# Kernel tuning notes

Measured on AMD Instinct MI355X. Metric: run time of the kernel, lower is better.

Reference implementation:

```python
import jax, jax.numpy as jnp
import numpy as np

NUM_HEADS = 20


def _rope(t, pos):
    """Rotary embedding (ESM style, rotate_half on full head_dim).
    t: (T, h, d), pos: (T,) float32 position within each sequence."""
    d = t.shape[-1]
    inv_freq = 1.0 / (10000.0 ** (jnp.arange(0, d, 2, dtype=jnp.float32) / d))  # (d/2,)
    freqs = pos[:, None] * inv_freq[None, :]          # (T, d/2)
    emb = jnp.concatenate([freqs, freqs], axis=-1)    # (T, d)
    cos = jnp.cos(emb)[:, None, :]                    # (T, 1, d)
    sin = jnp.sin(emb)[:, None, :]
    x1, x2 = jnp.split(t, 2, axis=-1)
    rot = jnp.concatenate([-x2, x1], axis=-1)
    return t * cos + rot * sin


def setup_inputs() -> dict:
    key = jax.random.key(0)
    ks = jax.random.split(key, 8)
    E = 1280
    lengths = np.array([512, 768, 1024, 1024, 1024, 1280, 1280, 1280], dtype=np.int64)
    cu_lens = jnp.asarray(np.concatenate([[0], np.cumsum(lengths)]).astype(np.int32))
    T = int(lengths.sum())  # 8192
    s = (2.0 / (E + E)) ** 0.5  # xavier-ish scale
    return {
        "x": jax.random.normal(ks[0], (T, E), jnp.float32),
        "cu_lens": cu_lens,
        "max_len": 1280,
        "Wq": jax.random.normal(ks[1], (E, E), jnp.float32) * s,
        "bq": jnp.zeros((E,), jnp.float32),
        "Wk": jax.random.normal(ks[2], (E, E), jnp.float32) * s,
        "bk": jnp.zeros((E,), jnp.float32),
        "Wv": jax.random.normal(ks[3], (E, E), jnp.float32) * s,
        "bv": jnp.zeros((E,), jnp.float32),
        "Wo": jax.random.normal(ks[4], (E, E), jnp.float32) * (2.0 ** 0.5) * s,
        "bo": jnp.zeros((E,), jnp.float32),
    }


def reference(x, cu_lens, max_len, Wq, bq, Wk, bk, Wv, bv, Wo, bo):
    T, E = x.shape
    h = NUM_HEADS
    d = E // h
    scale = d ** -0.5
    # fused QKV projections (q pre-scaled, softmax_scale=1 as in the original)
    q = ((x @ Wq.T + bq) * scale).reshape(T, h, d)
    k = (x @ Wk.T + bk).reshape(T, h, d)
    v = (x @ Wv.T + bv).reshape(T, h, d)
    # per-token sequence id and within-sequence position from cu_lens
    t_idx = jnp.arange(T)
    seq_id = jnp.searchsorted(cu_lens, t_idx, side='right') - 1  # (T,)
    pos = t_idx - cu_lens[seq_id]                                # (T,) int
    # rotary on q and k with per-sequence positions
    posf = pos.astype(jnp.float32)
    q = _rope(q, posf)
    k = _rope(k, posf)
    # scatter packed tokens into padded (B, max_len, h, d) layout
    B = cu_lens.shape[0] - 1
    qp = jnp.zeros((B, max_len, h, d), q.dtype).at[seq_id, pos].set(q)
    kp = jnp.zeros((B, max_len, h, d), k.dtype).at[seq_id, pos].set(k)
    vp = jnp.zeros((B, max_len, h, d), v.dtype).at[seq_id, pos].set(v)
    valid = jnp.zeros((B, max_len), bool).at[seq_id, pos].set(True)
    # non-causal attention within each sequence (block-diagonal over packed tokens)
    scores = jnp.einsum('blhd,bmhd->bhlm', qp, kp)
    scores = jnp.where(valid[:, None, None, :], scores, -1e9)
    attn = jax.nn.softmax(scores, axis=-1)
    o = jnp.einsum('bhlm,bmhd->blhd', attn, vp)
    # gather back to packed layout and apply output projection
    out_tok = o[seq_id, pos].reshape(T, E)
    return out_tok @ Wo.T + bo
```

## Files before the change

### kernel.cpp

```cpp
#include <hip/hip_runtime.h>
#include <hip/hip_bf16.h>
#include <cstdint>

#define E_DIM   1280
#define NHEADS  20
#define HDIM    64
#define QKV_LD  3840

typedef __attribute__((ext_vector_type(8))) short bf8_t;
typedef __attribute__((ext_vector_type(4))) short bf4_t;
typedef __attribute__((ext_vector_type(4))) float f4_t;

__device__ __forceinline__ short f2bs(float f) {
    union { __hip_bfloat16 h; short s; } u;
    u.h = __float2bfloat16(f);
    return u.s;
}

__device__ __forceinline__ bf4_t pk4(f4_t s) {
    union { bf4_t v; uint32_t u[2]; } r;
    asm("v_cvt_pk_bf16_f32 %0, %1, %2" : "=v"(r.u[0]) : "v"(s[0]), "v"(s[1]));
    asm("v_cvt_pk_bf16_f32 %0, %1, %2" : "=v"(r.u[1]) : "v"(s[2]), "v"(s[3]));
    return r.v;
}

__device__ __forceinline__ f4_t mfma16x32(bf8_t a, bf8_t b, f4_t c) {
    return __builtin_amdgcn_mfma_f32_16x16x32_bf16(a, b, c, 0, 0, 0);
}
__device__ __forceinline__ f4_t mfma16x16(bf4_t a, bf4_t b, f4_t c) {
    return __builtin_amdgcn_mfma_f32_16x16x16bf16_1k(a, b, c, 0, 0, 0);
}

__device__ __forceinline__ void gl_lds16(const void* g, void* l) {
    auto gp = reinterpret_cast<__attribute__((address_space(1))) unsigned int*>(
        reinterpret_cast<uintptr_t>(g));
    auto lp = reinterpret_cast<__attribute__((address_space(3))) unsigned int*>(
        reinterpret_cast<uintptr_t>(l));
    __builtin_amdgcn_global_load_lds(gp, lp, 16, 0, 0);
}

#define QSCALE 0.18033688011112042f

__device__ __forceinline__ void cvt8(__hip_bfloat16* dst, const float* src, float sc) {
    float4 a = *(const float4*)src;
    float4 b = *(const float4*)(src + 4);
    bf8_t v;
    v[0] = f2bs(a.x * sc); v[1] = f2bs(a.y * sc); v[2] = f2bs(a.z * sc); v[3] = f2bs(a.w * sc);
    v[4] = f2bs(b.x * sc); v[5] = f2bs(b.y * sc); v[6] = f2bs(b.z * sc); v[7] = f2bs(b.w * sc);
    *(bf8_t*)dst = v;
}

__global__ __launch_bounds__(256) void prep_kernel(
    const float* __restrict__ x,
    const float* __restrict__ wq, const float* __restrict__ wk,
    const float* __restrict__ wv, const float* __restrict__ wo,
    const float* __restrict__ bq, const float* __restrict__ bk, const float* __restrict__ bv,
    __hip_bfloat16* __restrict__ xbf, __hip_bfloat16* __restrict__ wqkv,
    __hip_bfloat16* __restrict__ wobf, float* __restrict__ bqkv,
    long nx8, long nw8, long nb8)
{
    long u = (long)blockIdx.x * 256 + threadIdx.x;
    if (u < nx8) { cvt8(xbf + u * 8, x + u * 8, 1.0f); return; }
    u -= nx8;
    if (u < 3 * nw8) {
        long e = u * 8;
        long w1 = nw8 * 8;
        const float* src; float sc;
        if (e < w1)            { src = wq + e;           sc = QSCALE; }
        else if (e < 2 * w1)   { src = wk + (e - w1);    sc = 1.0f; }
        else                   { src = wv + (e - 2*w1);  sc = 1.0f; }
        cvt8(wqkv + e, src, sc);
        return;
    }
    u -= 3 * nw8;
    if (u < nw8) { cvt8(wobf + u * 8, wo + u * 8, 1.0f); return; }
    u -= nw8;
    if (u < nb8) {
        long e = u * 8;
        #pragma unroll
        for (int j = 0; j < 8; j++) {
            long i = e + j;
            float v;
            if (i < E_DIM)           v = bq[i] * QSCALE;
            else if (i < 2 * E_DIM)  v = bk[i - E_DIM];
            else                     v = bv[i - 2 * E_DIM];
            bqkv[i] = v;
        }
    }
}

template<bool BF16_OUT>
__global__ __launch_bounds__(256, 3) void gemm_nt(
    const __hip_bfloat16* __restrict__ A, const __hip_bfloat16* __restrict__ Bw,
    const float* __restrict__ bias, void* __restrict__ Cout,
    int M, int N, int K, int ldc)
{
    __shared__ __align__(16) __hip_bfloat16 As[128 * 32];
    __shared__ __align__(16) __hip_bfloat16 Bs[128 * 32];
    const int t = threadIdx.x;
    const int wv = t >> 6;
    const int ln = t & 63;
    const int m16 = ln & 15, q4 = ln >> 4;
    const int row0 = blockIdx.y * 128, col0 = blockIdx.x * 128;
    const int wm = (wv >> 1) * 64, wn = (wv & 1) * 64;

    f4_t acc[4][4] = {};

    for (int k0 = 0; k0 < K; k0 += 32) {
        #pragma unroll
        for (int i = 0; i < 2; i++) {
            int s = i * 256 + t;
            int r = s >> 2, c = s & 3;
            gl_lds16(A + (size_t)(row0 + r) * K + k0 + c * 8,
                     As + (size_t)(i * 256 + wv * 64) * 8);
        }
        #pragma unroll
        for (int i = 0; i < 2; i++) {
            int s = i * 256 + t;
            int r = s >> 2, c = s & 3;
            gl_lds16(Bw + (size_t)(col0 + r) * K + k0 + c * 8,
                     Bs + (size_t)(i * 256 + wv * 64) * 8);
        }
        __syncthreads();
        bf8_t af[4], bfr[4];
        #pragma unroll
        for (int mt = 0; mt < 4; mt++)
            af[mt] = *(const bf8_t*)&As[(wm + mt * 16 + m16) * 32 + q4 * 8];
        #pragma unroll
        for (int nt = 0; nt < 4; nt++)
            bfr[nt] = *(const bf8_t*)&Bs[(wn + nt * 16 + m16) * 32 + q4 * 8];
        #pragma unroll
        for (int mt = 0; mt < 4; mt++)
            #pragma unroll
            for (int nt = 0; nt < 4; nt++)
                acc[mt][nt] = mfma16x32(af[mt], bfr[nt], acc[mt][nt]);
        __syncthreads();
    }

    #pragma unroll
    for (int nt = 0; nt < 4; nt++) {
        int cg = col0 + wn + nt * 16 + m16;
        float bv = bias[cg];
        #pragma unroll
        for (int mt = 0; mt < 4; mt++) {
            #pragma unroll
            for (int r = 0; r < 4; r++) {
                int rg = row0 + wm + mt * 16 + q4 * 4 + r;
                float v = acc[mt][nt][r] + bv;
                if constexpr (BF16_OUT)
                    ((__hip_bfloat16*)Cout)[(long)rg * ldc + cg] = __float2bfloat16(v);
                else
                    ((float*)Cout)[(long)rg * ldc + cg] = v;
            }
        }
    }
}

__global__ __launch_bounds__(512, 2) void gemm256(
    const __hip_bfloat16* __restrict__ A, const __hip_bfloat16* __restrict__ Bw,
    const float* __restrict__ bias, __hip_bfloat16* __restrict__ Cout,
    __hip_bfloat16* __restrict__ vtout, int Tdim,
    int M, int N, int K, int ldc)
{
    __shared__ __align__(16) __hip_bfloat16 As[2][256 * 64];
    __shared__ __align__(16) __hip_bfloat16 Bs[2][256 * 64];

    const int t = threadIdx.x;
    const int wv = t >> 6, ln = t & 63;
    const int m16 = ln & 15, q4 = ln >> 4;
    const int wr = wv >> 2, wc = wv & 3;

    const int gx = N >> 8;
    const int nwg = gridDim.x;
    const int id = blockIdx.x;
    const int swz = ((nwg & 7) == 0) ? (id & 7) * (nwg >> 3) + (id >> 3) : id;
    const int col0 = (swz % gx) << 8;
    const int row0 = (swz / gx) << 8;

    const int NT = K >> 6;

    auto stage = [&](const __hip_bfloat16* src, __hip_bfloat16* dst) {
        #pragma unroll
        for (int i = 0; i < 4; i++) {
            int s = i * 512 + t;
            int r = s >> 3, c = (s & 7) ^ (r & 7);
            gl_lds16(src + (size_t)r * K + c * 8,
                     (char*)dst + (size_t)(i * 512 + wv * 64) * 16);
        }
    };

    stage(A  + (size_t)row0 * K,      &As[0][0]);
    stage(Bw + (size_t)col0 * K,      &Bs[0][0]);
    if (NT > 1) {
        stage(A  + (size_t)row0 * K + 64, &As[1][0]);
        stage(Bw + (size_t)col0 * K + 64, &Bs[1][0]);
        asm volatile("s_waitcnt vmcnt(8)" ::: "memory");
    } else {
        asm volatile("s_waitcnt vmcnt(0)" ::: "memory");
    }
    __builtin_amdgcn_s_barrier();

    f4_t acc[8][4] = {};

    for (int kt = 0; kt < NT; kt++) {
        const __hip_bfloat16* Ab = &As[kt & 1][0];
        const __hip_bfloat16* Bb = &Bs[kt & 1][0];

        auto lda = [&](const __hip_bfloat16* base, int r, int kc) {
            return *(const bf8_t*)&base[r * 64 + ((((kc << 2) | q4) ^ (r & 7)) << 3)];
        };

        bf8_t afr[4][2], bf0[2][2], bf1[2][2];
        #pragma unroll
        for (int mt = 0; mt < 4; mt++)
            #pragma unroll
            for (int kc = 0; kc < 2; kc++)
                afr[mt][kc] = lda(Ab, wr * 128 + mt * 16 + m16, kc);
        #pragma unroll
        for (int nt = 0; nt < 2; nt++)
            #pragma unroll
            for (int kc = 0; kc < 2; kc++)
                bf0[nt][kc] = lda(Bb, wc * 64 + nt * 16 + m16, kc);

        __builtin_amdgcn_s_setprio(1);
        #pragma unroll
        for (int mt = 0; mt < 4; mt++)
            #pragma unroll
            for (int nt = 0; nt < 2; nt++)
                #pragma unroll
                for (int kc = 0; kc < 2; kc++)
                    acc[mt][nt] = mfma16x32(afr[mt][kc], bf0[nt][kc], acc[mt][nt]);
        __builtin_amdgcn_s_setprio(0);

        #pragma unroll
        for (int nt = 0; nt < 2; nt++)
            #pragma unroll
            for (int kc = 0; kc < 2; kc++)
                bf1[nt][kc] = lda(Bb, wc * 64 + (2 + nt) * 16 + m16, kc);

        __builtin_amdgcn_s_setprio(1);
        #pragma unroll
        for (int mt = 0; mt < 4; mt++)
            #pragma unroll
            for (int nt = 0; nt < 2; nt++)
                #pragma unroll
                for (int kc = 0; kc < 2; kc++)
                    acc[mt][2 + nt] = mfma16x32(afr[mt][kc], bf1[nt][kc], acc[mt][2 + nt]);
        __builtin_amdgcn_s_setprio(0);

        #pragma unroll
        for (int mt = 0; mt < 4; mt++)
            #pragma unroll
            for (int kc = 0; kc < 2; kc++)
                afr[mt][kc] = lda(Ab, wr * 128 + (4 + mt) * 16 + m16, kc);

        __builtin_amdgcn_s_setprio(1);
        #pragma unroll
        for (int mt = 0; mt < 4; mt++)
            #pragma unroll
            for (int nt = 0; nt < 2; nt++)
                #pragma unroll
                for (int kc = 0; kc < 2; kc++)
                    acc[4 + mt][2 + nt] = mfma16x32(afr[mt][kc], bf1[nt][kc], acc[4 + mt][2 + nt]);
        __builtin_amdgcn_s_setprio(0);

        __builtin_amdgcn_s_setprio(1);
        #pragma unroll
        for (int mt = 0; mt < 4; mt++)
            #pragma unroll
            for (int nt = 0; nt < 2; nt++)
                #pragma unroll
                for (int kc = 0; kc < 2; kc++)
                    acc[4 + mt][nt] = mfma16x32(afr[mt][kc], bf0[nt][kc], acc[4 + mt][nt]);
        __builtin_amdgcn_s_setprio(0);

        asm volatile("s_waitcnt lgkmcnt(0)" ::: "memory");
        __builtin_amdgcn_s_barrier();

        if (kt + 2 < NT) {
            stage(A  + (size_t)row0 * K + (size_t)(kt + 2) * 64, &As[kt & 1][0]);
            stage(Bw + (size_t)col0 * K + (size_t)(kt + 2) * 64, &Bs[kt & 1][0]);
        }
        if (kt + 1 < NT) {
            if (kt + 2 < NT)
                asm volatile("s_waitcnt vmcnt(8)" ::: "memory");
            else
                asm volatile("s_waitcnt vmcnt(0)" ::: "memory");
            __builtin_amdgcn_s_barrier();
        }
    }

    if (col0 >= 2 * E_DIM) {
        #pragma unroll
        for (int nt = 0; nt < 4; nt++) {
            int cg = col0 + wc * 64 + nt * 16 + m16;
            float bval = bias[cg];
            int vrow = cg - 2 * E_DIM;
            #pragma unroll
            for (int mt = 0; mt < 8; mt++) {
                int rg0 = row0 + wr * 128 + mt * 16 + q4 * 4;
                f4_t vv;
                #pragma unroll
                for (int r = 0; r < 4; r++) vv[r] = acc[mt][nt][r] + bval;
                *(bf4_t*)&vtout[(long)vrow * Tdim + rg0] = pk4(vv);
            }
        }
    } else {
        #pragma unroll
        for (int nt = 0; nt < 4; nt++) {
            int cg = col0 + wc * 64 + nt * 16 + m16;
            float bval = bias[cg];
            #pragma unroll
            for (int mt = 0; mt < 8; mt++) {
                #pragma unroll
                for (int r = 0; r < 4; r++) {
                    int rg = row0 + wr * 128 + mt * 16 + q4 * 4 + r;
                    Cout[(long)rg * ldc + cg] = __float2bfloat16(acc[mt][nt][r] + bval);
                }
            }
        }
    }
}

__global__ __launch_bounds__(256) void rope_kernel(
    __hip_bfloat16* __restrict__ qkv, const int* __restrict__ cu, int B, int T)
{
    long idx = (long)blockIdx.x * 256 + threadIdx.x;
    int i = idx & 31;
    long r = idx >> 5;
    int h = (int)(r % NHEADS);
    int tok = (int)(r / NHEADS);
    if (tok >= T) return;
    int pos = tok;
    for (int b = 1; b <= B; b++) if (tok >= cu[b]) pos = tok - cu[b];
    float rev = (float)pos * exp2f(-(float)i * 0.41524100558003436f
                                   - 2.6514961294723187f);
    rev = rev - floorf(rev);
    float s, c;
    asm("v_sin_f32 %0, %1" : "=v"(s) : "v"(rev));
    asm("v_cos_f32 %0, %1" : "=v"(c) : "v"(rev));
    long base = (long)tok * QKV_LD + h * HDIM + i;
    {
        float q1 = __bfloat162float(qkv[base]);
        float q2 = __bfloat162float(qkv[base + 32]);
        qkv[base]      = __float2bfloat16(q1 * c - q2 * s);
        qkv[base + 32] = __float2bfloat16(q2 * c + q1 * s);
    }
    {
        long kb = base + E_DIM;
        float k1 = __bfloat162float(qkv[kb]);
        float k2 = __bfloat162float(qkv[kb + 32]);
        qkv[kb]      = __float2bfloat16(k1 * c - k2 * s);
        qkv[kb + 32] = __float2bfloat16(k2 * c + k1 * s);
    }
}

__global__ __launch_bounds__(256, 4) void attn_kernel(
    const __hip_bfloat16* __restrict__ qkv, const __hip_bfloat16* __restrict__ vt,
    const int* __restrict__ cu, __hip_bfloat16* __restrict__ obuf, int B, int T)
{
    __shared__ __align__(16) __hip_bfloat16 Ks[2][64 * 64];
    __shared__ __align__(16) __hip_bfloat16 Vs[2][64 * 64];

    int idx = blockIdx.x;
    int h = idx % NHEADS;
    int gt = idx / NHEADS;
    int b = B - 1, l = 0, seq0 = 0;
    for (; b >= 0; --b) {
        seq0 = cu[b];
        l = cu[b + 1] - seq0;
        int ntile = (l + 127) >> 7;
        if (gt < ntile) break;
        gt -= ntile;
    }
    if (b < 0) return;
    int q0 = gt * 128;
    const int NT = (l + 63) >> 6;

    const int t = threadIdx.x;
    const int wv = t >> 6, ln = t & 63;
    const int m16 = ln & 15, q4 = ln >> 4;

    auto stage_full = [&](int kv0n, int bi) {
        #pragma unroll
        for (int i = 0; i < 2; i++) {
            int s2 = i * 256 + t;
            int key = s2 >> 3, cg = (s2 & 7) ^ (key & 7);
            gl_lds16(qkv + (long)(seq0 + kv0n + key) * QKV_LD + E_DIM + h * HDIM + cg * 8,
                     (char*)&Ks[bi][0] + (size_t)(i * 256 + wv * 64) * 16);
        }
        #pragma unroll
        for (int i = 0; i < 2; i++) {
            int s2 = i * 256 + t;
            int d = s2 >> 3, cg = (s2 & 7) ^ (d & 7);
            gl_lds16(vt + (long)(h * HDIM + d) * T + seq0 + kv0n + cg * 8,
                     (char*)&Vs[bi][0] + (size_t)(i * 256 + wv * 64) * 16);
        }
    };
    auto stage_tail = [&](int kv0n, int bi) {
        #pragma unroll
        for (int i = 0; i < 2; i++) {
            int s2 = i * 256 + t;
            int key = s2 >> 3, c = s2 & 7;
            bf8_t v = (bf8_t)0;
            if (kv0n + key < l)
                v = *(const bf8_t*)(qkv + (long)(seq0 + kv0n + key) * QKV_LD + E_DIM + h * HDIM + c * 8);
            *(bf8_t*)&Ks[bi][key * 64 + (c ^ (key & 7)) * 8] = v;
        }
        #pragma unroll
        for (int i = 0; i < 2; i++) {
            int s2 = i * 256 + t;
            int d = s2 >> 3, c = s2 & 7;
            bf8_t v = (bf8_t)0;
            int tb = kv0n + c * 8;
            #pragma unroll
            for (int u = 0; u < 8; u++)
                if (tb + u < l)
                    v[u] = *(const short*)&vt[(long)(h * HDIM + d) * T + seq0 + tb + u];
            *(bf8_t*)&Vs[bi][d * 64 + (c ^ (d & 7)) * 8] = v;
        }
    };

    if (64 <= l) stage_full(0, 0); else stage_tail(0, 0);

    bf8_t bq[2][2];
    #pragma unroll
    for (int nt = 0; nt < 2; nt++) {
        int qrow = q0 + wv * 32 + nt * 16 + m16;
        #pragma unroll
        for (int kc = 0; kc < 2; kc++) {
            bf8_t v = (bf8_t)0;
            if (qrow < l)
                v = *(const bf8_t*)(qkv + (long)(seq0 + qrow) * QKV_LD + h * HDIM + kc * 32 + q4 * 8);
            bq[nt][kc] = v;
        }
    }

    f4_t oacc[2][4] = {};
    float m_s[2] = {-1e30f, -1e30f};
    float l_s[2] = {0.0f, 0.0f};

    const int ksw0 = (q4 ^ (m16 & 7)) * 8;
    const int ksw1 = ((4 + q4) ^ (m16 & 7)) * 8;

    asm volatile("s_waitcnt vmcnt(0) lgkmcnt(0)" ::: "memory");
    __builtin_amdgcn_s_barrier();

    for (int it = 0; it < NT; ++it) {
        const int kv0 = it << 6;
        const bool full = (kv0 + 64 <= l);
        if (it + 1 < NT) {
            int kvn = kv0 + 64;
            if (kvn + 64 <= l) stage_full(kvn, (it + 1) & 1);
            else stage_tail(kvn, (it + 1) & 1);
        }
        const __hip_bfloat16* Kb = Ks[it & 1];
        const __hip_bfloat16* Vb = Vs[it & 1];

        f4_t S[2][4];
        __builtin_amdgcn_s_setprio(1);
        #pragma unroll
        for (int mt = 0; mt < 4; mt++) {
            const __hip_bfloat16* krow = &Kb[(mt * 16 + m16) * 64];
            bf8_t ak0 = *(const bf8_t*)(krow + ksw0);
            bf8_t ak1 = *(const bf8_t*)(krow + ksw1);
            #pragma unroll
            for (int nt = 0; nt < 2; nt++) {
                f4_t a = {};
                a = mfma16x32(ak0, bq[nt][0], a);
                a = mfma16x32(ak1, bq[nt][1], a);
                S[nt][mt] = a;
            }
        }
        __builtin_amdgcn_s_setprio(0);

        if (!full) {
            #pragma unroll
            for (int mt = 0; mt < 4; mt++) {
                #pragma unroll
                for (int r = 0; r < 4; r++) {
                    bool valid = (kv0 + mt * 16 + q4 * 4 + r) < l;
                    #pragma unroll
                    for (int nt = 0; nt < 2; nt++)
                        if (!valid) S[nt][mt][r] = -1e30f;
                }
            }
        }

        #pragma unroll
        for (int nt = 0; nt < 2; nt++) {
            float pm[4];
            #pragma unroll
            for (int mt = 0; mt < 4; mt++)
                pm[mt] = fmaxf(fmaxf(S[nt][mt][0], S[nt][mt][1]),
                               fmaxf(S[nt][mt][2], S[nt][mt][3]));
            float mx = fmaxf(fmaxf(pm[0], pm[1]), fmaxf(pm[2], pm[3]));
            mx = fmaxf(mx, __shfl_xor(mx, 16));
            mx = fmaxf(mx, __shfl_xor(mx, 32));
            if (!__all(mx - m_s[nt] <= 8.0f)) {
                float mn = fmaxf(m_s[nt], mx);
                float al = exp2f(m_s[nt] - mn);
                m_s[nt] = mn;
                l_s[nt] *= al;
                #pragma unroll
                for (int dt = 0; dt < 4; dt++)
                    #pragma unroll
                    for (int r = 0; r < 4; r++)
                        oacc[nt][dt][r] *= al;
            }
            float mcur = m_s[nt];
            float ps[4];
            #pragma unroll
            for (int mt = 0; mt < 4; mt++) {
                f4_t p;
                p[0] = exp2f(S[nt][mt][0] - mcur);
                p[1] = exp2f(S[nt][mt][1] - mcur);
                p[2] = exp2f(S[nt][mt][2] - mcur);
                p[3] = exp2f(S[nt][mt][3] - mcur);
                S[nt][mt] = p;
                ps[mt] = (p[0] + p[1]) + (p[2] + p[3]);
            }
            l_s[nt] += (ps[0] + ps[1]) + (ps[2] + ps[3]);
        }

        __builtin_amdgcn_s_setprio(1);
        #pragma unroll
        for (int mt = 0; mt < 4; mt++) {
            bf4_t bp0 = pk4(S[0][mt]);
            bf4_t bp1 = pk4(S[1][mt]);
            const int vsw = ((mt * 2 + (q4 >> 1)) ^ (m16 & 7)) * 8 + (q4 & 1) * 4;
            #pragma unroll
            for (int dt = 0; dt < 4; dt++) {
                bf4_t av = *(const bf4_t*)&Vb[(dt * 16 + m16) * 64 + vsw];
                oacc[0][dt] = mfma16x16(av, bp0, oacc[0][dt]);
                oacc[1][dt] = mfma16x16(av, bp1, oacc[1][dt]);
            }
        }
        __builtin_amdgcn_s_setprio(0);

        if (it + 1 < NT) {
            asm volatile("s_waitcnt vmcnt(0) lgkmcnt(0)" ::: "memory");
            __builtin_amdgcn_s_barrier();
        }
    }

    #pragma unroll
    for (int nt = 0; nt < 2; nt++) {
        float ls = l_s[nt];
        ls += __shfl_xor(ls, 16);
        ls += __shfl_xor(ls, 32);
        float inv = 1.0f / ls;
        int qrow = q0 + wv * 32 + nt * 16 + m16;
        if (qrow < l) {
            #pragma unroll
            for (int dt = 0; dt < 4; dt++) {
                f4_t o;
                #pragma unroll
                for (int r = 0; r < 4; r++)
                    o[r] = oacc[nt][dt][r] * inv;
                *(bf4_t*)&obuf[(long)(seq0 + qrow) * E_DIM + h * HDIM + dt * 16 + q4 * 4] = pk4(o);
            }
        }
    }
}

extern "C" void kernel_launch(void* const* d_in, const int* in_sizes, int n_in,
                              void* d_out, int out_size, void* d_ws, size_t ws_size,
                              hipStream_t stream) {
    const int E = E_DIM;
    const int T = in_sizes[0] / E;
    const int B = in_sizes[1] - 1;

    const float* x  = (const float*)d_in[0];
    const int*   cu = (const int*)d_in[1];
    const float* Wq = (const float*)d_in[3];
    const float* bq = (const float*)d_in[4];
    const float* Wk = (const float*)d_in[5];
    const float* bk = (const float*)d_in[6];
    const float* Wv = (const float*)d_in[7];
    const float* bv = (const float*)d_in[8];
    const float* Wo = (const float*)d_in[9];
    const float* bo = (const float*)d_in[10];

    char* ws = (char*)d_ws;
    size_t off = 0;
    auto alloc = [&](size_t bytes) -> void* {
        void* p = ws + off;
        off = (off + bytes + 255) & ~(size_t)255;
        return p;
    };
    __hip_bfloat16* xbf   = (__hip_bfloat16*)alloc((size_t)T * E * 2);
    __hip_bfloat16* wqkv  = (__hip_bfloat16*)alloc((size_t)3 * E * E * 2);
    __hip_bfloat16* wobf  = (__hip_bfloat16*)alloc((size_t)E * E * 2);
    float*          bqkv  = (float*)alloc((size_t)3 * E * 4);
    __hip_bfloat16* qkvb  = (__hip_bfloat16*)alloc((size_t)T * 3 * E * 2);
    __hip_bfloat16* vt    = (__hip_bfloat16*)alloc((size_t)E * T * 2);
    __hip_bfloat16* obuf  = xbf;

    long nx8 = (long)T * E / 8;
    long nw8 = (long)E * E / 8;
    long nb8 = (long)3 * E / 8;
    long total = nx8 + 4 * nw8 + nb8;
    int pblocks = (int)((total + 255) / 256);
    prep_kernel<<<pblocks, 256, 0, stream>>>(x, Wq, Wk, Wv, Wo, bq, bk, bv,
                                             xbf, wqkv, wobf, bqkv, nx8, nw8, nb8);

    gemm256<<<(T / 256) * (3 * E / 256), 512, 0, stream>>>(
        xbf, wqkv, bqkv, qkvb, vt, T, T, 3 * E, E, 3 * E);

    rope_kernel<<<(int)(((long)T * NHEADS * 32) / 256), 256, 0, stream>>>(qkvb, cu, B, T);

    int qtiles_ub = T / 128 + B;
    attn_kernel<<<qtiles_ub * NHEADS, 256, 0, stream>>>(qkvb, vt, cu, obuf, B, T);

    gemm_nt<false><<<dim3(E / 128, T / 128), 256, 0, stream>>>(
        obuf, wobf, bo, d_out, T, E, E, E);
}
```

Before: 378.4 us.

## Split GEMM LDS tiles into half-buffers and interleave loads with MFMA phases

Splits the 256-row A and B shared-memory tiles into 128-row halves and issues the global-to-LDS load for each half between the MFMA phases of the current k-step, so the next tile streams in while compute runs. This replaces the bulk staging of the whole next tile after the compute block. The cost is extra workgroup barriers per iteration and more fragile waitcnt bookkeeping across the finer stages.

```diff
diff --git a/kernel.cpp b/kernel.cpp
--- a/kernel.cpp
+++ b/kernel.cpp
@@ -162,8 +162,8 @@
     __hip_bfloat16* __restrict__ vtout, int Tdim,
     int M, int N, int K, int ldc)
 {
-    __shared__ __align__(16) __hip_bfloat16 As[2][256 * 64];
-    __shared__ __align__(16) __hip_bfloat16 Bs[2][256 * 64];
+    __shared__ __align__(16) __hip_bfloat16 Ah[2][2][128 * 64];
+    __shared__ __align__(16) __hip_bfloat16 Bh[2][2][128 * 64];
 
     const int t = threadIdx.x;
     const int wv = t >> 6, ln = t & 63;
@@ -179,9 +179,18 @@
 
     const int NT = K >> 6;
 
-    auto stage = [&](const __hip_bfloat16* src, __hip_bfloat16* dst) {
-        #pragma unroll
-        for (int i = 0; i < 4; i++) {
+    auto stage_part = [&](int kt, int part) {
+        const __hip_bfloat16* src;
+        __hip_bfloat16* dst;
+        if (part < 2) {
+            src = A + (size_t)(row0 + part * 128) * K + (size_t)kt * 64;
+            dst = &Ah[kt & 1][part][0];
+        } else {
+            src = Bw + (size_t)(col0 + (part - 2) * 128) * K + (size_t)kt * 64;
+            dst = &Bh[kt & 1][part - 2][0];
+        }
+        #pragma unroll
+        for (int i = 0; i < 2; i++) {
             int s = i * 512 + t;
             int r = s >> 3, c = (s & 7) ^ (r & 7);
             gl_lds16(src + (size_t)r * K + c * 8,
@@ -189,12 +198,10 @@
         }
     };
 
-    stage(A  + (size_t)row0 * K,      &As[0][0]);
-    stage(Bw + (size_t)col0 * K,      &Bs[0][0]);
+    stage_part(0, 0); stage_part(0, 1); stage_part(0, 2); stage_part(0, 3);
     if (NT > 1) {
-        stage(A  + (size_t)row0 * K + 64, &As[1][0]);
-        stage(Bw + (size_t)col0 * K + 64, &Bs[1][0]);
-        asm volatile("s_waitcnt vmcnt(8)" ::: "memory");
+        stage_part(1, 0);
+        asm volatile("s_waitcnt vmcnt(2)" ::: "memory");
     } else {
         asm volatile("s_waitcnt vmcnt(0)" ::: "memory");
     }
@@ -203,25 +210,29 @@
     f4_t acc[8][4] = {};
 
     for (int kt = 0; kt < NT; kt++) {
-        const __hip_bfloat16* Ab = &As[kt & 1][0];
-        const __hip_bfloat16* Bb = &Bs[kt & 1][0];
+        const __hip_bfloat16* Ab = &Ah[kt & 1][wr][0];
+        const __hip_bfloat16* Bb = &Bh[kt & 1][wc >> 1][0];
+        const int bc0 = (wc & 1) * 64;
 
         auto lda = [&](const __hip_bfloat16* base, int r, int kc) {
             return *(const bf8_t*)&base[r * 64 + ((((kc << 2) | q4) ^ (r & 7)) << 3)];
         };
 
-        bf8_t afr[4][2], bf0[2][2], bf1[2][2];
+        bf8_t af[4][2], bf0[2][2], bf1[2][2];
+
         #pragma unroll
         for (int mt = 0; mt < 4; mt++)
             #pragma unroll
             for (int kc = 0; kc < 2; kc++)
-                afr[mt][kc] = lda(Ab, wr * 128 + mt * 16 + m16, kc);
+                af[mt][kc] = lda(Ab, mt * 16 + m16, kc);
         #pragma unroll
         for (int nt = 0; nt < 2; nt++)
             #pragma unroll
             for (int kc = 0; kc < 2; kc++)
-                bf0[nt][kc] = lda(Bb, wc * 64 + nt * 16 + m16, kc);
-
+                bf0[nt][kc] = lda(Bb, bc0 + nt * 16 + m16, kc);
+        if (kt + 1 < NT) stage_part(kt + 1, 1);
+        asm volatile("s_waitcnt lgkmcnt(8)" ::: "memory");
+        __builtin_amdgcn_s_barrier();
         __builtin_amdgcn_s_setprio(1);
         #pragma unroll
         for (int mt = 0; mt < 4; mt++)
@@ -229,15 +240,17 @@
             for (int nt = 0; nt < 2; nt++)
                 #pragma unroll
                 for (int kc = 0; kc < 2; kc++)
-                    acc[mt][nt] = mfma16x32(afr[mt][kc], bf0[nt][kc], acc[mt][nt]);
+                    acc[mt][nt] = mfma16x32(af[mt][kc], bf0[nt][kc], acc[mt][nt]);
         __builtin_amdgcn_s_setprio(0);
+        __builtin_amdgcn_s_barrier();
 
         #pragma unroll
         for (int nt = 0; nt < 2; nt++)
             #pragma unroll
             for (int kc = 0; kc < 2; kc++)
-                bf1[nt][kc] = lda(Bb, wc * 64 + (2 + nt) * 16 + m16, kc);
-
+                bf1[nt][kc] = lda(Bb, bc0 + (2 + nt) * 16 + m16, kc);
+        if (kt + 1 < NT) stage_part(kt + 1, 2);
+        __builtin_amdgcn_s_barrier();
         __builtin_amdgcn_s_setprio(1);
         #pragma unroll
         for (int mt = 0; mt < 4; mt++)
@@ -245,15 +258,17 @@
             for (int nt = 0; nt < 2; nt++)
                 #pragma unroll
                 for (int kc = 0; kc < 2; kc++)
-                    acc[mt][2 + nt] = mfma16x32(afr[mt][kc], bf1[nt][kc], acc[mt][2 + nt]);
+                    acc[mt][2 + nt] = mfma16x32(af[mt][kc], bf1[nt][kc], acc[mt][2 + nt]);
         __builtin_amdgcn_s_setprio(0);
+        __builtin_amdgcn_s_barrier();
 
         #pragma unroll
         for (int mt = 0; mt < 4; mt++)
             #pragma unroll
             for (int kc = 0; kc < 2; kc++)
-                afr[mt][kc] = lda(Ab, wr * 128 + (4 + mt) * 16 + m16, kc);
-
+                af[mt][kc] = lda(Ab, (4 + mt) * 16 + m16, kc);
+        if (kt + 1 < NT) stage_part(kt + 1, 3);
+        __builtin_amdgcn_s_barrier();
         __builtin_amdgcn_s_setprio(1);
         #pragma unroll
         for (int mt = 0; mt < 4; mt++)
@@ -261,33 +276,28 @@
             for (int nt = 0; nt < 2; nt++)
                 #pragma unroll
                 for (int kc = 0; kc < 2; kc++)
-                    acc[4 + mt][2 + nt] = mfma16x32(afr[mt][kc], bf1[nt][kc], acc[4 + mt][2 + nt]);
+                    acc[4 + mt][2 + nt] = mfma16x32(af[mt][kc], bf1[nt][kc], acc[4 + mt][2 + nt]);
         __builtin_amdgcn_s_setprio(0);
-
-        __builtin_amdgcn_s_setprio(1);
-        #pragma unroll
-        for (int mt = 0; mt < 4; mt++)
-            #pragma unroll
-            for (int nt = 0; nt < 2; nt++)
-                #pragma unroll
-                for (int kc = 0; kc < 2; kc++)
-                    acc[4 + mt][nt] = mfma16x32(afr[mt][kc], bf0[nt][kc], acc[4 + mt][nt]);
-        __builtin_amdgcn_s_setprio(0);
-
-        asm volatile("s_waitcnt lgkmcnt(0)" ::: "memory");
         __builtin_amdgcn_s_barrier();
 
-        if (kt + 2 < NT) {
-            stage(A  + (size_t)row0 * K + (size_t)(kt + 2) * 64, &As[kt & 1][0]);
-            stage(Bw + (size_t)col0 * K + (size_t)(kt + 2) * 64, &Bs[kt & 1][0]);
-        }
+        if (kt + 2 < NT) stage_part(kt + 2, 0);
         if (kt + 1 < NT) {
             if (kt + 2 < NT)
-                asm volatile("s_waitcnt vmcnt(8)" ::: "memory");
+                asm volatile("s_waitcnt vmcnt(2)" ::: "memory");
             else
                 asm volatile("s_waitcnt vmcnt(0)" ::: "memory");
-            __builtin_amdgcn_s_barrier();
-        }
+        }
+        __builtin_amdgcn_s_barrier();
+        __builtin_amdgcn_s_setprio(1);
+        #pragma unroll
+        for (int mt = 0; mt < 4; mt++)
+            #pragma unroll
+            for (int nt = 0; nt < 2; nt++)
+                #pragma unroll
+                for (int kc = 0; kc < 2; kc++)
+                    acc[4 + mt][nt] = mfma16x32(af[mt][kc], bf0[nt][kc], acc[4 + mt][nt]);
+        __builtin_amdgcn_s_setprio(0);
+        if (kt + 1 < NT) __builtin_amdgcn_s_barrier();
     }
 
     if (col0 >= 2 * E_DIM) {
```

New measurement: 373.2 us. About the same (-1.4%).
